# Kernel optimization log

Measured on AMD Instinct MI355X. Metric: run time of the kernel, lower is better.

The kernel has to match this reference:

```python
import jax, jax.numpy as jnp
import numpy as np

B, K, I, H = 32768, 4, 256, 256


def _linear_init(key, out_dim, in_dim, bias):
    # mimics torch nn.Linear default init: U(-1/sqrt(in), 1/sqrt(in))
    bound = 1.0 / np.sqrt(in_dim)
    kw, kb = jax.random.split(key)
    W = jax.random.uniform(kw, (out_dim, in_dim), minval=-bound, maxval=bound, dtype=jnp.float32)
    if bias:
        b = jax.random.uniform(kb, (out_dim,), minval=-bound, maxval=bound, dtype=jnp.float32)
        return W, b
    return W


def setup_inputs() -> dict:
    key = jax.random.key(0)
    ks = jax.random.split(key, 12)
    x = jax.random.normal(ks[0], (B, I), dtype=jnp.float32)
    child_x = jax.random.normal(ks[1], (B, K, I), dtype=jnp.float32)
    Wi, bi = _linear_init(ks[2], H, I, True)
    Wf, bf = _linear_init(ks[3], H, I, True)
    Wo, bo = _linear_init(ks[4], H, I, True)
    Wu, bu = _linear_init(ks[5], H, I, True)
    Ui = _linear_init(ks[6], H, H, False)
    Uo = _linear_init(ks[7], H, H, False)
    Uu = _linear_init(ks[8], H, H, False)
    # per-arity forget weights wf1..wfK, stacked [K, H, H]
    WfK = jnp.stack([_linear_init(jax.random.fold_in(ks[9], k), H, H, False) for k in range(K)])
    return dict(x=x, child_x=child_x, Wi=Wi, bi=bi, Wf=Wf, bf=bf, Wo=Wo, bo=bo,
                Wu=Wu, bu=bu, Ui=Ui, Uo=Uo, Uu=Uu, WfK=WfK)


def reference(x, child_x, Wi, bi, Wf, bf, Wo, bo, Wu, bu, Ui, Uo, Uu, WfK):
    # ---- leaf_forward on all K children, batched: [B, K, H] ----
    ci = jax.nn.sigmoid(child_x @ Wi.T + bi)
    co = jax.nn.sigmoid(child_x @ Wo.T + bo)
    cu = jnp.tanh(child_x @ Wu.T + bu)
    cc = ci * cu                      # child cell states [B, K, H]
    ch = co * jnp.tanh(cc)            # child hidden states [B, K, H]

    # ---- node_forward on root ----
    hsum = ch.sum(axis=1)             # sum_j h_j  [B, H]
    i = jax.nn.sigmoid(x @ Wi.T + bi + hsum @ Ui.T)
    # faithful quirk: f_k = sigmoid(Wf x + Wf_k @ (sum_j h_j))
    ukfh = jnp.einsum('bh,kgh->bkg', hsum, WfK)                 # [B, K, H]
    f = jax.nn.sigmoid((x @ Wf.T + bf)[:, None, :] + ukfh)       # [B, K, H]
    o = jax.nn.sigmoid(x @ Wo.T + bo + hsum @ Uo.T)
    u = jnp.tanh(x @ Wu.T + bu + hsum @ Uu.T)
    c = i * u + (f * cc).sum(axis=1)  # [B, H]
    h = o * jnp.tanh(c)
    return (h, c)
```

## Files before the change

### kernel.cpp

```cpp
#include <hip/hip_runtime.h>
#include <hip/hip_bf16.h>


#define BB 32768
#define KK 4
#define II 256
#define HH 256

typedef __bf16 bf16x8 __attribute__((ext_vector_type(8)));
typedef __bf16 bf16x4 __attribute__((ext_vector_type(4)));
typedef float f32x4 __attribute__((ext_vector_type(4)));

#define MFMA16(a, b, c) __builtin_amdgcn_mfma_f32_16x16x32_bf16(a, b, c, 0, 0, 0)

static __device__ __forceinline__ float fsig(float x) {
    return 1.0f / (1.0f + __expf(-x));
}
static __device__ __forceinline__ float ftanhf(float x) {
    float e = __expf(2.0f * x);
    return 1.0f - 2.0f / (e + 1.0f);
}

static __device__ __forceinline__ bf16x8 cvt8v(float4 f0, float4 f1) {
    bf16x8 v;
    v[0] = (__bf16)f0.x; v[1] = (__bf16)f0.y; v[2] = (__bf16)f0.z; v[3] = (__bf16)f0.w;
    v[4] = (__bf16)f1.x; v[5] = (__bf16)f1.y; v[6] = (__bf16)f1.z; v[7] = (__bf16)f1.w;
    return v;
}
static __device__ __forceinline__ bf16x8 cvt8(const float* __restrict__ p) {
    return cvt8v(((const float4*)p)[0], ((const float4*)p)[1]);
}

struct CvtArgs {
    const float* src[8];
    __bf16* dst[8];
    int n[8];
};
__global__ __launch_bounds__(256) void cvt_k(CvtArgs a) {
    const int t = blockIdx.y;
    const int i = (blockIdx.x * 256 + threadIdx.x) * 4;
    if (i < a.n[t]) {
        float4 f = *(const float4*)(a.src[t] + i);
        bf16x4 v;
        v[0] = (__bf16)f.x; v[1] = (__bf16)f.y; v[2] = (__bf16)f.z; v[3] = (__bf16)f.w;
        *(bf16x4*)(a.dst[t] + i) = v;
    }
}

#define ROWSTR 264
__global__ __launch_bounds__(512, 2) void child_gates_k(
    const float* __restrict__ child_x,
    const __bf16* __restrict__ Wi, const __bf16* __restrict__ Wo,
    const __bf16* __restrict__ Wu,
    const float* __restrict__ bi, const float* __restrict__ bo,
    const float* __restrict__ bu,
    __bf16* __restrict__ cc, __bf16* __restrict__ hsum)
{
    const int tid  = threadIdx.x;
    const int wave = tid >> 6;
    const int lane = tid & 63;
    const int l16  = lane & 15;
    const int quad = lane >> 4;
    const int rowchunk = blockIdx.x >> 1;
    const int ct   = (blockIdx.x & 1) * 8 + wave;
    const int n    = ct * 16 + l16;

    bf16x8 w[3][8];
    {
        const int base = n * II + quad * 8;
#pragma unroll
        for (int ks = 0; ks < 8; ++ks) {
            w[0][ks] = *(const bf16x8*)(Wi + base + ks * 32);
            w[1][ks] = *(const bf16x8*)(Wo + base + ks * 32);
            w[2][ks] = *(const bf16x8*)(Wu + base + ks * 32);
        }
    }
    const float bin = bi[n], bon = bo[n], bun = bu[n];

    __shared__ __bf16 As[2][16 * ROWSTR];

    const int srow = tid >> 5;
    const int scol = (tid & 31) * 8;
    const float* gbase = child_x + ((size_t)rowchunk * 256 + srow) * II + scol;

    float4 f0 = ((const float4*)gbase)[0];
    float4 f1 = ((const float4*)gbase)[1];
    *(bf16x8*)(&As[0][srow * ROWSTR + scol]) = cvt8v(f0, f1);
    __syncthreads();

    for (int t = 0; t < 16; ++t) {
        float4 g0, g1;
        if (t < 15) {
            const float* gp = gbase + (size_t)(t + 1) * 16 * II;
            g0 = ((const float4*)gp)[0];
            g1 = ((const float4*)gp)[1];
        }

        const __bf16* ap = &As[t & 1][l16 * ROWSTR + quad * 8];
        f32x4 ai = {0.f,0.f,0.f,0.f}, ao = {0.f,0.f,0.f,0.f}, au = {0.f,0.f,0.f,0.f};
#pragma unroll
        for (int ks = 0; ks < 8; ++ks) {
            bf16x8 a = *(const bf16x8*)(ap + ks * 32);
            ai = MFMA16(a, w[0][ks], ai);
            ao = MFMA16(a, w[1][ks], ao);
            au = MFMA16(a, w[2][ks], au);
        }

        {
            const int b = rowchunk * 64 + t * 4 + quad;
            float chs = 0.f;
            bf16x4 ccv4;
#pragma unroll
            for (int r = 0; r < 4; ++r) {
                float civ = fsig(ai[r] + bin);
                float cov = fsig(ao[r] + bon);
                float cuv = ftanhf(au[r] + bun);
                float ccv = civ * cuv;
                chs += cov * ftanhf(ccv);
                ccv4[r] = (__bf16)ccv;
            }
            *(bf16x4*)(cc + ((size_t)b * HH + n) * KK) = ccv4;
            hsum[(size_t)b * HH + n] = (__bf16)chs;
        }

        if (t < 15)
            *(bf16x8*)(&As[(t + 1) & 1][srow * ROWSTR + scol]) = cvt8v(g0, g1);
        __syncthreads();
    }
}

__global__ __launch_bounds__(256, 2) void root_k(
    const float* __restrict__ x,
    const __bf16* __restrict__ Wi, const __bf16* __restrict__ Wf,
    const __bf16* __restrict__ Wo, const __bf16* __restrict__ Wu,
    const __bf16* __restrict__ Ui, const __bf16* __restrict__ Uo,
    const __bf16* __restrict__ Uu, const __bf16* __restrict__ WfK,
    const float* __restrict__ bi, const float* __restrict__ bf_,
    const float* __restrict__ bo, const float* __restrict__ bu,
    const __bf16* __restrict__ cc, const __bf16* __restrict__ hsum,
    float* __restrict__ out)
{
    const int tid  = threadIdx.x;
    const int lane = tid & 63;
    const int wave = tid >> 6;
    const int l16  = lane & 15;
    const int quad = lane >> 4;
    const int row0 = blockIdx.x * 64;
    const int ct   = blockIdx.y * 4 + wave;
    const int n    = ct * 16 + l16;

    __shared__ __bf16 xs[64 * 256];
    __shared__ __bf16 hsl[64 * 256];

    {
        const float* xg = x + (size_t)row0 * II;
#pragma unroll
        for (int p = 0; p < 16; ++p) {
            const int e = p * 1024 + tid * 4;
            float4 f = *(const float4*)(xg + e);
            bf16x4 v;
            v[0] = (__bf16)f.x; v[1] = (__bf16)f.y;
            v[2] = (__bf16)f.z; v[3] = (__bf16)f.w;
            const int r = e >> 8, c = e & 255;
            int off = r * 512 + c * 2;
            off ^= (r & 7) << 4;
            *(bf16x4*)((char*)xs + off) = v;
        }
        const __bf16* hg = hsum + (size_t)row0 * HH;
#pragma unroll
        for (int p = 0; p < 8; ++p) {
            const int u = p * 256 + tid;
            bf16x8 v = *(const bf16x8*)(hg + u * 8);
            const int r = u >> 5, c = (u & 31) * 8;
            int off = r * 512 + c * 2;
            off ^= (r & 7) << 4;
            *(bf16x8*)((char*)hsl + off) = v;
        }
    }
    __syncthreads();

    const float bin = bi[n], bfn = bf_[n], bon = bo[n], bun = bu[n];
    const int wo = n * II + quad * 8;
    const int cbase = quad * 8;

#define LDA(plane, rt, ks) \
    (*(const bf16x8*)((const char*)(plane) + \
        ((((rt) * 16 + l16) * 512 + ((cbase) + (ks) * 32) * 2) ^ \
         ((((rt) * 16 + l16) & 7) << 4))))

    f32x4 ai[4], ao[4], au[4];
    {
        const f32x4 z = {0.f, 0.f, 0.f, 0.f};
#pragma unroll
        for (int rt = 0; rt < 4; ++rt) { ai[rt] = z; ao[rt] = z; au[rt] = z; }
    }
#pragma unroll
    for (int ks = 0; ks < 8; ++ks) {
        const int o = wo + ks * 32;
        bf16x8 bwi = *(const bf16x8*)(Wi + o);
        bf16x8 bui = *(const bf16x8*)(Ui + o);
        bf16x8 bwo = *(const bf16x8*)(Wo + o);
        bf16x8 buo = *(const bf16x8*)(Uo + o);
        bf16x8 bwu = *(const bf16x8*)(Wu + o);
        bf16x8 buu = *(const bf16x8*)(Uu + o);
#pragma unroll
        for (int rt = 0; rt < 4; ++rt) {
            bf16x8 a = LDA(xs, rt, ks);
            bf16x8 h = LDA(hsl, rt, ks);
            ai[rt] = MFMA16(a, bwi, ai[rt]);
            ai[rt] = MFMA16(h, bui, ai[rt]);
            ao[rt] = MFMA16(a, bwo, ao[rt]);
            ao[rt] = MFMA16(h, buo, ao[rt]);
            au[rt] = MFMA16(a, bwu, au[rt]);
            au[rt] = MFMA16(h, buu, au[rt]);
        }
    }
    f32x4 cpart[4], ovv[4];
#pragma unroll
    for (int rt = 0; rt < 4; ++rt)
#pragma unroll
        for (int r = 0; r < 4; ++r) {
            const float iv = fsig(ai[rt][r] + bin);
            const float ov = fsig(ao[rt][r] + bon);
            const float uv = ftanhf(au[rt][r] + bun);
            cpart[rt][r] = iv * uv;
            ovv[rt][r]   = ov;
        }

#pragma unroll
    for (int h2 = 0; h2 < 2; ++h2) {
        bf16x4 cv4[2][4];
#pragma unroll
        for (int rt2 = 0; rt2 < 2; ++rt2)
#pragma unroll
            for (int r = 0; r < 4; ++r) {
                const int b = row0 + (h2 * 2 + rt2) * 16 + quad * 4 + r;
                cv4[rt2][r] = *(const bf16x4*)(cc + ((size_t)b * HH + n) * KK);
            }

        f32x4 axf[2], af0[2], af1[2], af2[2], af3[2];
        {
            const f32x4 z = {0.f, 0.f, 0.f, 0.f};
#pragma unroll
            for (int rt2 = 0; rt2 < 2; ++rt2) {
                axf[rt2] = z; af0[rt2] = z; af1[rt2] = z;
                af2[rt2] = z; af3[rt2] = z;
            }
        }
#pragma unroll
        for (int ks = 0; ks < 8; ++ks) {
            const int o = wo + ks * 32;
            bf16x8 bwf = *(const bf16x8*)(Wf + o);
            bf16x8 bk0 = *(const bf16x8*)(WfK + 0 * HH * II + o);
            bf16x8 bk1 = *(const bf16x8*)(WfK + 1 * HH * II + o);
            bf16x8 bk2 = *(const bf16x8*)(WfK + 2 * HH * II + o);
            bf16x8 bk3 = *(const bf16x8*)(WfK + 3 * HH * II + o);
#pragma unroll
            for (int rt2 = 0; rt2 < 2; ++rt2) {
                const int rt = h2 * 2 + rt2;
                bf16x8 a = LDA(xs, rt, ks);
                bf16x8 h = LDA(hsl, rt, ks);
                axf[rt2] = MFMA16(a, bwf, axf[rt2]);
                af0[rt2] = MFMA16(h, bk0, af0[rt2]);
                af1[rt2] = MFMA16(h, bk1, af1[rt2]);
                af2[rt2] = MFMA16(h, bk2, af2[rt2]);
                af3[rt2] = MFMA16(h, bk3, af3[rt2]);
            }
        }

#pragma unroll
        for (int rt2 = 0; rt2 < 2; ++rt2) {
            const int rt = h2 * 2 + rt2;
#pragma unroll
            for (int r = 0; r < 4; ++r) {
                const int b = row0 + rt * 16 + quad * 4 + r;
                const float xfv = axf[rt2][r] + bfn;
                float cv = cpart[rt][r];
                cv += fsig(xfv + af0[rt2][r]) * (float)cv4[rt2][r][0];
                cv += fsig(xfv + af1[rt2][r]) * (float)cv4[rt2][r][1];
                cv += fsig(xfv + af2[rt2][r]) * (float)cv4[rt2][r][2];
                cv += fsig(xfv + af3[rt2][r]) * (float)cv4[rt2][r][3];
                const float hv = ovv[rt][r] * ftanhf(cv);
                out[(size_t)b * HH + n] = hv;
                out[(size_t)BB * HH + (size_t)b * HH + n] = cv;
            }
        }
    }
#undef LDA
}

extern "C" void kernel_launch(void* const* d_in, const int* in_sizes, int n_in,
                              void* d_out, int out_size, void* d_ws, size_t ws_size,
                              hipStream_t stream) {
    const float* x    = (const float*)d_in[0];
    const float* cx   = (const float*)d_in[1];
    const float* Wi   = (const float*)d_in[2];
    const float* bi   = (const float*)d_in[3];
    const float* Wf   = (const float*)d_in[4];
    const float* bf_  = (const float*)d_in[5];
    const float* Wo   = (const float*)d_in[6];
    const float* bo   = (const float*)d_in[7];
    const float* Wu   = (const float*)d_in[8];
    const float* bu   = (const float*)d_in[9];
    const float* Ui   = (const float*)d_in[10];
    const float* Uo   = (const float*)d_in[11];
    const float* Uu   = (const float*)d_in[12];
    const float* WfK  = (const float*)d_in[13];

    __bf16* cc = (__bf16*)d_ws;
    __bf16* hs = cc + (size_t)BB * KK * HH;
    __bf16* wb = hs + (size_t)BB * HH;
    __bf16 *Wi_b = wb,            *Wf_b = Wi_b + HH * II, *Wo_b = Wf_b + HH * II,
           *Wu_b = Wo_b + HH * II, *Ui_b = Wu_b + HH * II, *Uo_b = Ui_b + HH * HH,
           *Uu_b = Uo_b + HH * HH, *WfK_b = Uu_b + HH * HH;

    CvtArgs ca;
    ca.src[0] = Wi;  ca.dst[0] = Wi_b;  ca.n[0] = HH * II;
    ca.src[1] = Wf;  ca.dst[1] = Wf_b;  ca.n[1] = HH * II;
    ca.src[2] = Wo;  ca.dst[2] = Wo_b;  ca.n[2] = HH * II;
    ca.src[3] = Wu;  ca.dst[3] = Wu_b;  ca.n[3] = HH * II;
    ca.src[4] = Ui;  ca.dst[4] = Ui_b;  ca.n[4] = HH * HH;
    ca.src[5] = Uo;  ca.dst[5] = Uo_b;  ca.n[5] = HH * HH;
    ca.src[6] = Uu;  ca.dst[6] = Uu_b;  ca.n[6] = HH * HH;
    ca.src[7] = WfK; ca.dst[7] = WfK_b; ca.n[7] = KK * HH * HH;

    cvt_k<<<dim3(KK * HH * HH / 1024, 8), dim3(256), 0, stream>>>(ca);
    child_gates_k<<<dim3(1024), dim3(512), 0, stream>>>(
        cx, Wi_b, Wo_b, Wu_b, bi, bo, bu, cc, hs);
    root_k<<<dim3(BB / 64, 4), dim3(256), 0, stream>>>(
        x, Wi_b, Wf_b, Wo_b, Wu_b, Ui_b, Uo_b, Uu_b, WfK_b,
        bi, bf_, bo, bu, cc, hs, (float*)d_out);
}
```

Before: 493.5 us.

## Restructure child kernel to load a 64-row tile once and widen root blocks

The child gates kernel no longer keeps weights resident in registers while looping over 16 double-buffered row chunks. Each block now converts a 64-row tile of child_x into swizzled shared memory in one pass and streams weight fragments from global memory across four row tiles, launching four times as many blocks. The root kernel moves to 512-thread blocks covering 8 column tiles, so each x/hsum tile is staged once per 128 columns instead of once per 64. The aim is more parallelism and fewer restaging passes, at the cost of more global weight reads and larger per-block shared memory, which limits occupancy.

```diff
diff --git a/kernel.cpp b/kernel.cpp
--- a/kernel.cpp
+++ b/kernel.cpp
@@ -19,16 +19,6 @@
 static __device__ __forceinline__ float ftanhf(float x) {
     float e = __expf(2.0f * x);
     return 1.0f - 2.0f / (e + 1.0f);
-}
-
-static __device__ __forceinline__ bf16x8 cvt8v(float4 f0, float4 f1) {
-    bf16x8 v;
-    v[0] = (__bf16)f0.x; v[1] = (__bf16)f0.y; v[2] = (__bf16)f0.z; v[3] = (__bf16)f0.w;
-    v[4] = (__bf16)f1.x; v[5] = (__bf16)f1.y; v[6] = (__bf16)f1.z; v[7] = (__bf16)f1.w;
-    return v;
-}
-static __device__ __forceinline__ bf16x8 cvt8(const float* __restrict__ p) {
-    return cvt8v(((const float4*)p)[0], ((const float4*)p)[1]);
 }
 
 struct CvtArgs {
@@ -47,8 +37,12 @@
     }
 }
 
-#define ROWSTR 264
-__global__ __launch_bounds__(512, 2) void child_gates_k(
+#define LDA(plane, rt, ks) \
+    (*(const bf16x8*)((const char*)(plane) + \
+        ((((rt) * 16 + l16) * 512 + (cbase + (ks) * 32) * 2) ^ \
+         ((((rt) * 16 + l16) & 7) << 4))))
+
+__global__ __launch_bounds__(512, 4) void child_gates_k(
     const float* __restrict__ child_x,
     const __bf16* __restrict__ Wi, const __bf16* __restrict__ Wo,
     const __bf16* __restrict__ Wu,
@@ -57,79 +51,80 @@
     __bf16* __restrict__ cc, __bf16* __restrict__ hsum)
 {
     const int tid  = threadIdx.x;
+    const int lane = tid & 63;
     const int wave = tid >> 6;
-    const int lane = tid & 63;
     const int l16  = lane & 15;
     const int quad = lane >> 4;
-    const int rowchunk = blockIdx.x >> 1;
-    const int ct   = (blockIdx.x & 1) * 8 + wave;
+    const int rowblock = blockIdx.x >> 1;
+    const int cg   = blockIdx.x & 1;
+    const int crbase = rowblock * 64;
+    const int ct   = cg * 8 + wave;
     const int n    = ct * 16 + l16;
 
-    bf16x8 w[3][8];
+    __shared__ __bf16 as_[64 * 256];
+
     {
-        const int base = n * II + quad * 8;
-#pragma unroll
-        for (int ks = 0; ks < 8; ++ks) {
-            w[0][ks] = *(const bf16x8*)(Wi + base + ks * 32);
-            w[1][ks] = *(const bf16x8*)(Wo + base + ks * 32);
-            w[2][ks] = *(const bf16x8*)(Wu + base + ks * 32);
-        }
-    }
+        const float* g = child_x + (size_t)crbase * II;
+#pragma unroll
+        for (int p = 0; p < 8; ++p) {
+            const int e = p * 2048 + tid * 4;
+            float4 f = *(const float4*)(g + e);
+            bf16x4 v;
+            v[0] = (__bf16)f.x; v[1] = (__bf16)f.y;
+            v[2] = (__bf16)f.z; v[3] = (__bf16)f.w;
+            const int r = e >> 8, c = e & 255;
+            int off = r * 512 + c * 2;
+            off ^= (r & 7) << 4;
+            *(bf16x4*)((char*)as_ + off) = v;
+        }
+    }
+    __syncthreads();
+
     const float bin = bi[n], bon = bo[n], bun = bu[n];
-
-    __shared__ __bf16 As[2][16 * ROWSTR];
-
-    const int srow = tid >> 5;
-    const int scol = (tid & 31) * 8;
-    const float* gbase = child_x + ((size_t)rowchunk * 256 + srow) * II + scol;
-
-    float4 f0 = ((const float4*)gbase)[0];
-    float4 f1 = ((const float4*)gbase)[1];
-    *(bf16x8*)(&As[0][srow * ROWSTR + scol]) = cvt8v(f0, f1);
-    __syncthreads();
-
-    for (int t = 0; t < 16; ++t) {
-        float4 g0, g1;
-        if (t < 15) {
-            const float* gp = gbase + (size_t)(t + 1) * 16 * II;
-            g0 = ((const float4*)gp)[0];
-            g1 = ((const float4*)gp)[1];
-        }
-
-        const __bf16* ap = &As[t & 1][l16 * ROWSTR + quad * 8];
-        f32x4 ai = {0.f,0.f,0.f,0.f}, ao = {0.f,0.f,0.f,0.f}, au = {0.f,0.f,0.f,0.f};
-#pragma unroll
-        for (int ks = 0; ks < 8; ++ks) {
-            bf16x8 a = *(const bf16x8*)(ap + ks * 32);
-            ai = MFMA16(a, w[0][ks], ai);
-            ao = MFMA16(a, w[1][ks], ao);
-            au = MFMA16(a, w[2][ks], au);
-        }
-
-        {
-            const int b = rowchunk * 64 + t * 4 + quad;
-            float chs = 0.f;
-            bf16x4 ccv4;
-#pragma unroll
-            for (int r = 0; r < 4; ++r) {
-                float civ = fsig(ai[r] + bin);
-                float cov = fsig(ao[r] + bon);
-                float cuv = ftanhf(au[r] + bun);
-                float ccv = civ * cuv;
-                chs += cov * ftanhf(ccv);
-                ccv4[r] = (__bf16)ccv;
-            }
-            *(bf16x4*)(cc + ((size_t)b * HH + n) * KK) = ccv4;
-            hsum[(size_t)b * HH + n] = (__bf16)chs;
-        }
-
-        if (t < 15)
-            *(bf16x8*)(&As[(t + 1) & 1][srow * ROWSTR + scol]) = cvt8v(g0, g1);
-        __syncthreads();
-    }
-}
-
-__global__ __launch_bounds__(256, 2) void root_k(
+    const int wo = n * II + quad * 8;
+    const int cbase = quad * 8;
+
+    f32x4 ai[4], ao[4], au[4];
+    {
+        const f32x4 z = {0.f, 0.f, 0.f, 0.f};
+#pragma unroll
+        for (int rt = 0; rt < 4; ++rt) { ai[rt] = z; ao[rt] = z; au[rt] = z; }
+    }
+#pragma unroll
+    for (int ks = 0; ks < 8; ++ks) {
+        const int o = wo + ks * 32;
+        bf16x8 bwi = *(const bf16x8*)(Wi + o);
+        bf16x8 bwo = *(const bf16x8*)(Wo + o);
+        bf16x8 bwu = *(const bf16x8*)(Wu + o);
+#pragma unroll
+        for (int rt = 0; rt < 4; ++rt) {
+            bf16x8 a = LDA(as_, rt, ks);
+            ai[rt] = MFMA16(a, bwi, ai[rt]);
+            ao[rt] = MFMA16(a, bwo, ao[rt]);
+            au[rt] = MFMA16(a, bwu, au[rt]);
+        }
+    }
+
+#pragma unroll
+    for (int rt = 0; rt < 4; ++rt) {
+        const int b = rowblock * 16 + rt * 4 + quad;
+        float chs = 0.f;
+        bf16x4 ccv4;
+#pragma unroll
+        for (int r = 0; r < 4; ++r) {
+            float civ = fsig(ai[rt][r] + bin);
+            float cov = fsig(ao[rt][r] + bon);
+            float cuv = ftanhf(au[rt][r] + bun);
+            float ccv = civ * cuv;
+            chs += cov * ftanhf(ccv);
+            ccv4[r] = (__bf16)ccv;
+        }
+        *(bf16x4*)(cc + ((size_t)b * HH + n) * KK) = ccv4;
+        hsum[(size_t)b * HH + n] = (__bf16)chs;
+    }
+}
+
+__global__ __launch_bounds__(512, 4) void root_k(
     const float* __restrict__ x,
     const __bf16* __restrict__ Wi, const __bf16* __restrict__ Wf,
     const __bf16* __restrict__ Wo, const __bf16* __restrict__ Wu,
@@ -146,7 +141,7 @@
     const int l16  = lane & 15;
     const int quad = lane >> 4;
     const int row0 = blockIdx.x * 64;
-    const int ct   = blockIdx.y * 4 + wave;
+    const int ct   = blockIdx.y * 8 + wave;
     const int n    = ct * 16 + l16;
 
     __shared__ __bf16 xs[64 * 256];
@@ -155,8 +150,8 @@
     {
         const float* xg = x + (size_t)row0 * II;
 #pragma unroll
-        for (int p = 0; p < 16; ++p) {
-            const int e = p * 1024 + tid * 4;
+        for (int p = 0; p < 8; ++p) {
+            const int e = p * 2048 + tid * 4;
             float4 f = *(const float4*)(xg + e);
             bf16x4 v;
             v[0] = (__bf16)f.x; v[1] = (__bf16)f.y;
@@ -168,8 +163,8 @@
         }
         const __bf16* hg = hsum + (size_t)row0 * HH;
 #pragma unroll
-        for (int p = 0; p < 8; ++p) {
-            const int u = p * 256 + tid;
+        for (int p = 0; p < 4; ++p) {
+            const int u = p * 512 + tid;
             bf16x8 v = *(const bf16x8*)(hg + u * 8);
             const int r = u >> 5, c = (u & 31) * 8;
             int off = r * 512 + c * 2;
@@ -182,11 +177,6 @@
     const float bin = bi[n], bfn = bf_[n], bon = bo[n], bun = bu[n];
     const int wo = n * II + quad * 8;
     const int cbase = quad * 8;
-
-#define LDA(plane, rt, ks) \
-    (*(const bf16x8*)((const char*)(plane) + \
-        ((((rt) * 16 + l16) * 512 + ((cbase) + (ks) * 32) * 2) ^ \
-         ((((rt) * 16 + l16) & 7) << 4))))
 
     f32x4 ai[4], ao[4], au[4];
     {
@@ -286,7 +276,6 @@
             }
         }
     }
-#undef LDA
 }
 
 extern "C" void kernel_launch(void* const* d_in, const int* in_sizes, int n_in,
@@ -325,9 +314,9 @@
     ca.src[7] = WfK; ca.dst[7] = WfK_b; ca.n[7] = KK * HH * HH;
 
     cvt_k<<<dim3(KK * HH * HH / 1024, 8), dim3(256), 0, stream>>>(ca);
-    child_gates_k<<<dim3(1024), dim3(512), 0, stream>>>(
+    child_gates_k<<<dim3(4096), dim3(512), 0, stream>>>(
         cx, Wi_b, Wo_b, Wu_b, bi, bo, bu, cc, hs);
-    root_k<<<dim3(BB / 64, 4), dim3(256), 0, stream>>>(
+    root_k<<<dim3(BB / 64, 2), dim3(512), 0, stream>>>(
         x, Wi_b, Wf_b, Wo_b, Wu_b, Ui_b, Uo_b, Uu_b, WfK_b,
         bi, bf_, bo, bu, cc, hs, (float*)d_out);
 }
```

Result: slower. 643.5 us (+30.4%).
